# Performance work log

Hardware: AMD Instinct MI355X
Metric: run time of the kernel (lower is better)

The kernel has to match this reference:

```python
import jax, jax.numpy as jnp
import numpy as np

V, DW, DH, OUT = 50000, 300, 50, 4
B, T = 1024, 200


def setup_inputs() -> dict:
    key = jax.random.key(0)
    ks = jax.random.split(key, 9)
    x = jax.random.randint(ks[0], (B, T), 0, V)
    lengs = jax.random.randint(ks[1], (B,), 1, T + 1)  # valid lengths >= 1
    k = 1.0 / np.sqrt(DH)
    emb = jax.random.normal(ks[2], (V, DW), jnp.float32)
    emb = emb.at[0].set(0.0)  # padding_idx=0
    w_ih = jax.random.uniform(ks[3], (4 * DH, DW), jnp.float32, -k, k)
    w_hh = jax.random.uniform(ks[4], (4 * DH, DH), jnp.float32, -k, k)
    b_ih = jax.random.uniform(ks[5], (4 * DH,), jnp.float32, -k, k)
    b_hh = jax.random.uniform(ks[6], (4 * DH,), jnp.float32, -k, k)
    w_out = jax.random.uniform(ks[7], (OUT, DH), jnp.float32, -k, k)
    b_out = jax.random.uniform(ks[8], (OUT,), jnp.float32, -k, k)
    return {"x": x, "lengs": lengs, "emb": emb, "w_ih": w_ih, "w_hh": w_hh,
            "b_ih": b_ih, "b_hh": b_hh, "w_out": w_out, "b_out": b_out}


def reference(x, lengs, emb, w_ih, w_hh, b_ih, b_hh, w_out, b_out):
    b, t = x.shape
    xe = emb[x]                                        # [B,T,DW]
    mask = jnp.arange(t)[None, :] < lengs[:, None]     # [B,T] valid steps
    bias = b_ih + b_hh                                 # [4*DH]

    def step(carry, inp):
        h, c = carry
        x_t, m_t = inp                                 # [B,DW], [B]
        g = x_t @ w_ih.T + h @ w_hh.T + bias           # [B,4*DH]
        i, f, gg, o = jnp.split(g, 4, axis=-1)         # torch gate order i,f,g,o
        c_new = jax.nn.sigmoid(f) * c + jax.nn.sigmoid(i) * jnp.tanh(gg)
        h_new = jax.nn.sigmoid(o) * jnp.tanh(c_new)
        m = m_t[:, None]
        # packed-sequence semantics: state frozen past each sequence's length
        return (jnp.where(m, h_new, h), jnp.where(m, c_new, c)), None

    h0 = jnp.zeros((b, DH), xe.dtype)
    (h, _), _ = jax.lax.scan(step, (h0, h0),
                             (xe.transpose(1, 0, 2), mask.T))
    logits = h @ w_out.T + b_out                       # hidden.view(B,-1) -> Linear
    return jax.nn.softmax(logits, axis=1)
```

## Files before the change

kernel.cpp:

```cpp
#include <hip/hip_runtime.h>
#include <math.h>

#define VOCAB 50000
#define DW 300
#define DH 50
#define G4 200
#define BATCH 1024
#define TMAX 200
#define OUTC 4

__global__ __launch_bounds__(256) void transpose_wih(
    const float* __restrict__ w_ih, float* __restrict__ w_T)
{
    int i = blockIdx.x * 256 + threadIdx.x;
    if (i < G4 * DW) {
        int u = i / DW, k = i % DW;
        int u2 = (u % DH) * 4 + (u / DH);
        w_T[k * G4 + u2] = w_ih[i];
    }
}

__global__ __launch_bounds__(256, 2) void proj_kernel(
    const float* __restrict__ emb, const float* __restrict__ w_T,
    const float* __restrict__ b_ih, const float* __restrict__ b_hh,
    float* __restrict__ emb_proj)
{
    __shared__ __align__(16) float e_s[100 * 108];
    const int tid = threadIdx.x;
    const int v0 = blockIdx.x * 100;
    const int m_idx = tid / 25;
    const int n_idx = tid % 25;

    float acc[10][8];
#pragma unroll
    for (int m = 0; m < 10; m++)
#pragma unroll
        for (int c = 0; c < 8; c++) acc[m][c] = 0.f;

    const float* wcol = w_T + n_idx * 8;

    for (int kc = 0; kc < DW; kc += 100) {
        __syncthreads();
        for (int i = tid; i < 2500; i += 256) {
            int r = i / 25, c = i % 25;
            float4 v = *(const float4*)&emb[(size_t)(v0 + r) * DW + kc + c * 4];
            *(float4*)&e_s[r * 108 + c * 4] = v;
        }
        __syncthreads();

        if (tid < 250) {
            float4 wa[4], wb[4];
#pragma unroll
            for (int j = 0; j < 4; j++) {
                const float* p = wcol + (size_t)(kc + j) * G4;
                wa[j] = *(const float4*)p;
                wb[j] = *(const float4*)(p + 4);
            }
            for (int kk = 0; kk < 25; kk++) {
                float4 na[4], nb[4];
                int kn = kc + ((kk < 24) ? (kk + 1) : kk) * 4;
#pragma unroll
                for (int j = 0; j < 4; j++) {
                    const float* p = wcol + (size_t)(kn + j) * G4;
                    na[j] = *(const float4*)p;
                    nb[j] = *(const float4*)(p + 4);
                }
                float4 e4[10];
#pragma unroll
                for (int m = 0; m < 10; m++)
                    e4[m] = *(const float4*)&e_s[(m_idx * 10 + m) * 108 + kk * 4];
#pragma unroll
                for (int j = 0; j < 4; j++) {
#pragma unroll
                    for (int m = 0; m < 10; m++) {
                        float ev = (j == 0) ? e4[m].x : (j == 1) ? e4[m].y
                                 : (j == 2) ? e4[m].z : e4[m].w;
                        acc[m][0] = fmaf(ev, wa[j].x, acc[m][0]);
                        acc[m][1] = fmaf(ev, wa[j].y, acc[m][1]);
                        acc[m][2] = fmaf(ev, wa[j].z, acc[m][2]);
                        acc[m][3] = fmaf(ev, wa[j].w, acc[m][3]);
                        acc[m][4] = fmaf(ev, wb[j].x, acc[m][4]);
                        acc[m][5] = fmaf(ev, wb[j].y, acc[m][5]);
                        acc[m][6] = fmaf(ev, wb[j].z, acc[m][6]);
                        acc[m][7] = fmaf(ev, wb[j].w, acc[m][7]);
                    }
                }
#pragma unroll
                for (int j = 0; j < 4; j++) { wa[j] = na[j]; wb[j] = nb[j]; }
            }
        }
    }

    if (tid < 250) {
        float bias[8];
#pragma unroll
        for (int c = 0; c < 8; c++) {
            int u2 = n_idx * 8 + c;
            int u  = (u2 & 3) * DH + (u2 >> 2);
            bias[c] = b_ih[u] + b_hh[u];
        }
#pragma unroll
        for (int m = 0; m < 10; m++) {
            float* dst = &emb_proj[(size_t)(v0 + m_idx * 10 + m) * G4 + n_idx * 8];
            *(float4*)dst = make_float4(acc[m][0] + bias[0], acc[m][1] + bias[1],
                                        acc[m][2] + bias[2], acc[m][3] + bias[3]);
            *(float4*)(dst + 4) = make_float4(acc[m][4] + bias[4], acc[m][5] + bias[5],
                                              acc[m][6] + bias[6], acc[m][7] + bias[7]);
        }
    }
}

template <int CTRL>
__device__ __forceinline__ float qbcast(float x) {
    return __int_as_float(__builtin_amdgcn_update_dpp(
        0, __float_as_int(x), CTRL, 0xF, 0xF, true));
}

__global__ __launch_bounds__(256, 2) void lstm_kernel(
    const int* __restrict__ x, const int* __restrict__ lengs,
    const float* __restrict__ emb_proj, const float* __restrict__ w_hh,
    const float* __restrict__ w_out, const float* __restrict__ b_out,
    float* __restrict__ out)
{
    __shared__ __align__(16) float hbuf[2][52];
    __shared__ int x_s[TMAX];
    __shared__ float red[OUTC];

    const int tid  = threadIdx.x;
    const int b    = blockIdx.x;
    const int gate = tid & 3;
    const int unit = tid >> 2;
    const int uu   = (unit < DH) ? unit : DH - 1;
    const int col  = (tid < G4) ? tid : 0;
    const int len  = lengs[b];

    for (int i = tid; i < TMAX; i += 256) x_s[i] = x[b * TMAX + i];
    if (tid < 52) hbuf[0][tid] = 0.f;

    const float* wr = w_hh + (size_t)(gate * DH + uu) * DH;
#define LDW(J) ({ float2 ta_ = *(const float2*)(wr + 4 * (J));                \
                  float2 tb_ = *(const float2*)(wr + 4 * (J) + 2);            \
                  make_float4(ta_.x, ta_.y, tb_.x, tb_.y); })
    const float4 W0 = LDW(0),  W1 = LDW(1),  W2  = LDW(2),  W3  = LDW(3);
    const float4 W4 = LDW(4),  W5 = LDW(5),  W6  = LDW(6),  W7  = LDW(7);
    const float4 W8 = LDW(8),  W9 = LDW(9),  W10 = LDW(10), W11 = LDW(11);
    const float2 W12 = *(const float2*)(wr + 48);
#undef LDW

    __syncthreads();

    const float* ep = emb_proj;
    float p0 = ep[(size_t)x_s[0] * G4 + col];
    float p1 = ep[(size_t)x_s[1] * G4 + col];
    float p2 = ep[(size_t)x_s[2] * G4 + col];
    float c_reg = 0.f;

    for (int t = 0; t < len; t++) {
        float cur = p0; p0 = p1; p1 = p2;
        int nt = t + 3; nt = (nt < TMAX) ? nt : TMAX - 1;
        p2 = ep[(size_t)x_s[nt] * G4 + col];

        const float* hb = hbuf[t & 1];
        float4 h0  = *(const float4*)(hb + 0);
        float4 h1  = *(const float4*)(hb + 4);
        float4 h2  = *(const float4*)(hb + 8);
        float4 h3  = *(const float4*)(hb + 12);
        float4 h4  = *(const float4*)(hb + 16);
        float4 h5  = *(const float4*)(hb + 20);
        float4 h6  = *(const float4*)(hb + 24);
        float4 h7  = *(const float4*)(hb + 28);
        float4 h8  = *(const float4*)(hb + 32);
        float4 h9  = *(const float4*)(hb + 36);
        float4 h10 = *(const float4*)(hb + 40);
        float4 h11 = *(const float4*)(hb + 44);
        float2 h12 = *(const float2*)(hb + 48);

#define DOT4(A, H, W)                                                         \
        A = fmaf((H).x, (W).x, fmaf((H).y, (W).y,                             \
            fmaf((H).z, (W).z, fmaf((H).w, (W).w, A))));
        float a0 = cur, a1 = 0.f, a2 = 0.f, a3 = 0.f;
        DOT4(a0, h0, W0)  DOT4(a1, h1, W1)  DOT4(a2, h2,  W2)  DOT4(a3, h3,  W3)
        DOT4(a0, h4, W4)  DOT4(a1, h5, W5)  DOT4(a2, h6,  W6)  DOT4(a3, h7,  W7)
        DOT4(a0, h8, W8)  DOT4(a1, h9, W9)  DOT4(a2, h10, W10) DOT4(a3, h11, W11)
        a1 = fmaf(h12.x, W12.x, fmaf(h12.y, W12.y, a1));
#undef DOT4
        float g = (a0 + a1) + (a2 + a3);

        const bool isg = (gate == 2);
        float arg = isg ? (-2.f * g) : (-g);
        float r   = 1.f / (1.f + __expf(arg));
        float v   = isg ? fmaf(2.f, r, -1.f) : r;

        float si = qbcast<0x00>(v);
        float sf = qbcast<0x55>(v);
        float tc = qbcast<0xAA>(v);
        float so = qbcast<0xFF>(v);

        float cn = fmaf(sf, c_reg, si * tc);
        c_reg = cn;
        float th = fmaf(2.f, 1.f / (1.f + __expf(-2.f * cn)), -1.f);
        float hn = so * th;
        if ((gate == 0) && (tid < G4)) hbuf[(t + 1) & 1][unit] = hn;
        __syncthreads();
    }

    const float* hf = hbuf[len & 1];
    if (tid < OUTC) {
        float lg = b_out[tid];
        const float* wo = w_out + tid * DH;
#pragma unroll
        for (int k = 0; k < DH; k++) lg = fmaf(hf[k], wo[k], lg);
        red[tid] = lg;
    }
    if (tid < OUTC) {
        float m = fmaxf(fmaxf(red[0], red[1]), fmaxf(red[2], red[3]));
        float s = 0.f;
#pragma unroll
        for (int j = 0; j < OUTC; j++) s += __expf(red[j] - m);
        out[b * OUTC + tid] = __expf(red[tid] - m) / s;
    }
}

extern "C" void kernel_launch(void* const* d_in, const int* in_sizes, int n_in,
                              void* d_out, int out_size, void* d_ws, size_t ws_size,
                              hipStream_t stream) {
    const int*   x     = (const int*)d_in[0];
    const int*   lengs = (const int*)d_in[1];
    const float* emb   = (const float*)d_in[2];
    const float* w_ih  = (const float*)d_in[3];
    const float* w_hh  = (const float*)d_in[4];
    const float* b_ih  = (const float*)d_in[5];
    const float* b_hh  = (const float*)d_in[6];
    const float* w_out = (const float*)d_in[7];
    const float* b_out = (const float*)d_in[8];
    float* out = (float*)d_out;

    float* emb_proj = (float*)d_ws;
    float* w_T      = emb_proj + (size_t)VOCAB * G4;

    hipLaunchKernelGGL(transpose_wih, dim3((G4 * DW + 255) / 256), dim3(256),
                       0, stream, w_ih, w_T);
    hipLaunchKernelGGL(proj_kernel, dim3(VOCAB / 100), dim3(256), 0, stream,
                       emb, w_T, b_ih, b_hh, emb_proj);
    hipLaunchKernelGGL(lstm_kernel, dim3(BATCH), dim3(256), 0, stream,
                       x, lengs, emb_proj, w_hh, w_out, b_out, out);
}
```

Measured before the change: 347.5 us.

## Process four batch sequences per block with masked steps and padded W_hh rows

Each LSTM block now runs four sequences in lockstep up to the longest of the four lengths. Per-sequence masks freeze the cell and hidden state once a sequence has ended. A small new kernel copies W_hh into a 52-float padded row layout so each row loads as aligned float4s. The goal is to share one barrier per timestep across four sequences and to give each thread independent work it can overlap. In exchange, only a quarter as many blocks are launched, which lowers occupancy. Sequences shorter than the longest in their group also do wasted steps.

```diff
diff --git a/kernel.cpp b/kernel.cpp
--- a/kernel.cpp
+++ b/kernel.cpp
@@ -8,6 +8,7 @@
 #define BATCH 1024
 #define TMAX 200
 #define OUTC 4
+#define NB 4
 
 __global__ __launch_bounds__(256) void transpose_wih(
     const float* __restrict__ w_ih, float* __restrict__ w_T)
@@ -110,114 +111,156 @@
     }
 }
 
+__global__ __launch_bounds__(256) void prep_whh(
+    const float* __restrict__ w_hh, float* __restrict__ wp)
+{
+    int r = threadIdx.x;
+    if (r < G4) {
+        int gate = r & 3, unit = r >> 2;
+        const float* src = w_hh + (size_t)(gate * DH + unit) * DH;
+        float* dst = wp + r * 52;
+        for (int k = 0; k < DH; k++) dst[k] = src[k];
+        dst[50] = 0.f; dst[51] = 0.f;
+    }
+}
+
 template <int CTRL>
 __device__ __forceinline__ float qbcast(float x) {
     return __int_as_float(__builtin_amdgcn_update_dpp(
         0, __float_as_int(x), CTRL, 0xF, 0xF, true));
 }
 
-__global__ __launch_bounds__(256, 2) void lstm_kernel(
+__global__ __launch_bounds__(256) void lstm_kernel(
     const int* __restrict__ x, const int* __restrict__ lengs,
-    const float* __restrict__ emb_proj, const float* __restrict__ w_hh,
+    const float* __restrict__ emb_proj, const float* __restrict__ wp,
     const float* __restrict__ w_out, const float* __restrict__ b_out,
     float* __restrict__ out)
 {
-    __shared__ __align__(16) float hbuf[2][52];
-    __shared__ int x_s[TMAX];
-    __shared__ float red[OUTC];
+    __shared__ __align__(16) float hbuf[2][NB][52];
+    __shared__ int x_s[NB][TMAX];
+    __shared__ float red[NB][OUTC];
 
     const int tid  = threadIdx.x;
-    const int b    = blockIdx.x;
+    const int b4   = blockIdx.x * NB;
     const int gate = tid & 3;
     const int unit = tid >> 2;
-    const int uu   = (unit < DH) ? unit : DH - 1;
-    const int col  = (tid < G4) ? tid : 0;
-    const int len  = lengs[b];
-
-    for (int i = tid; i < TMAX; i += 256) x_s[i] = x[b * TMAX + i];
-    if (tid < 52) hbuf[0][tid] = 0.f;
-
-    const float* wr = w_hh + (size_t)(gate * DH + uu) * DH;
-#define LDW(J) ({ float2 ta_ = *(const float2*)(wr + 4 * (J));                \
-                  float2 tb_ = *(const float2*)(wr + 4 * (J) + 2);            \
-                  make_float4(ta_.x, ta_.y, tb_.x, tb_.y); })
-    const float4 W0 = LDW(0),  W1 = LDW(1),  W2  = LDW(2),  W3  = LDW(3);
-    const float4 W4 = LDW(4),  W5 = LDW(5),  W6  = LDW(6),  W7  = LDW(7);
-    const float4 W8 = LDW(8),  W9 = LDW(9),  W10 = LDW(10), W11 = LDW(11);
-    const float2 W12 = *(const float2*)(wr + 48);
-#undef LDW
+    const int row  = (tid < G4) ? tid : 0;
+
+    for (int i = tid; i < NB * TMAX; i += 256) {
+        int nb = i / TMAX, tt = i % TMAX;
+        x_s[nb][tt] = x[(size_t)(b4 + nb) * TMAX + tt];
+    }
+    for (int i = tid; i < 2 * NB * 52; i += 256) ((float*)hbuf)[i] = 0.f;
+
+    const int len0 = lengs[b4 + 0];
+    const int len1 = lengs[b4 + 1];
+    const int len2 = lengs[b4 + 2];
+    const int len3 = lengs[b4 + 3];
+    const int lenmax = max(max(len0, len1), max(len2, len3));
+
+    const float* wr = wp + (size_t)row * 52;
+    const float4 W0  = *(const float4*)(wr + 0);
+    const float4 W1  = *(const float4*)(wr + 4);
+    const float4 W2  = *(const float4*)(wr + 8);
+    const float4 W3  = *(const float4*)(wr + 12);
+    const float4 W4  = *(const float4*)(wr + 16);
+    const float4 W5  = *(const float4*)(wr + 20);
+    const float4 W6  = *(const float4*)(wr + 24);
+    const float4 W7  = *(const float4*)(wr + 28);
+    const float4 W8  = *(const float4*)(wr + 32);
+    const float4 W9  = *(const float4*)(wr + 36);
+    const float4 W10 = *(const float4*)(wr + 40);
+    const float4 W11 = *(const float4*)(wr + 44);
+    const float4 W12 = *(const float4*)(wr + 48);
 
     __syncthreads();
 
     const float* ep = emb_proj;
-    float p0 = ep[(size_t)x_s[0] * G4 + col];
-    float p1 = ep[(size_t)x_s[1] * G4 + col];
-    float p2 = ep[(size_t)x_s[2] * G4 + col];
-    float c_reg = 0.f;
-
-    for (int t = 0; t < len; t++) {
-        float cur = p0; p0 = p1; p1 = p2;
-        int nt = t + 3; nt = (nt < TMAX) ? nt : TMAX - 1;
-        p2 = ep[(size_t)x_s[nt] * G4 + col];
-
-        const float* hb = hbuf[t & 1];
-        float4 h0  = *(const float4*)(hb + 0);
-        float4 h1  = *(const float4*)(hb + 4);
-        float4 h2  = *(const float4*)(hb + 8);
-        float4 h3  = *(const float4*)(hb + 12);
-        float4 h4  = *(const float4*)(hb + 16);
-        float4 h5  = *(const float4*)(hb + 20);
-        float4 h6  = *(const float4*)(hb + 24);
-        float4 h7  = *(const float4*)(hb + 28);
-        float4 h8  = *(const float4*)(hb + 32);
-        float4 h9  = *(const float4*)(hb + 36);
-        float4 h10 = *(const float4*)(hb + 40);
-        float4 h11 = *(const float4*)(hb + 44);
-        float2 h12 = *(const float2*)(hb + 48);
+    float p00 = ep[(size_t)x_s[0][0] * G4 + row];
+    float p01 = ep[(size_t)x_s[0][1] * G4 + row];
+    float p10 = ep[(size_t)x_s[1][0] * G4 + row];
+    float p11 = ep[(size_t)x_s[1][1] * G4 + row];
+    float p20 = ep[(size_t)x_s[2][0] * G4 + row];
+    float p21 = ep[(size_t)x_s[2][1] * G4 + row];
+    float p30 = ep[(size_t)x_s[3][0] * G4 + row];
+    float p31 = ep[(size_t)x_s[3][1] * G4 + row];
+    float c0 = 0.f, c1 = 0.f, c2 = 0.f, c3 = 0.f;
+    float hp0 = 0.f, hp1 = 0.f, hp2 = 0.f, hp3 = 0.f;
 
 #define DOT4(A, H, W)                                                         \
         A = fmaf((H).x, (W).x, fmaf((H).y, (W).y,                             \
             fmaf((H).z, (W).z, fmaf((H).w, (W).w, A))));
-        float a0 = cur, a1 = 0.f, a2 = 0.f, a3 = 0.f;
-        DOT4(a0, h0, W0)  DOT4(a1, h1, W1)  DOT4(a2, h2,  W2)  DOT4(a3, h3,  W3)
-        DOT4(a0, h4, W4)  DOT4(a1, h5, W5)  DOT4(a2, h6,  W6)  DOT4(a3, h7,  W7)
-        DOT4(a0, h8, W8)  DOT4(a1, h9, W9)  DOT4(a2, h10, W10) DOT4(a3, h11, W11)
-        a1 = fmaf(h12.x, W12.x, fmaf(h12.y, W12.y, a1));
+
+#define STEP_ROW(R, pR0, pR1, cR, hpR, lenR)                                  \
+    {                                                                         \
+        float cur = pR0; pR0 = pR1;                                           \
+        pR1 = ep[(size_t)x_s[R][nt] * G4 + row];                              \
+        const float* hb = &hbuf[t & 1][R][0];                                 \
+        float4 h0  = *(const float4*)(hb + 0);                                \
+        float4 h1  = *(const float4*)(hb + 4);                                \
+        float4 h2  = *(const float4*)(hb + 8);                                \
+        float4 h3  = *(const float4*)(hb + 12);                               \
+        float4 h4  = *(const float4*)(hb + 16);                               \
+        float4 h5  = *(const float4*)(hb + 20);                               \
+        float4 h6  = *(const float4*)(hb + 24);                               \
+        float4 h7  = *(const float4*)(hb + 28);                               \
+        float4 h8  = *(const float4*)(hb + 32);                               \
+        float4 h9  = *(const float4*)(hb + 36);                               \
+        float4 h10 = *(const float4*)(hb + 40);                               \
+        float4 h11 = *(const float4*)(hb + 44);                               \
+        float4 h12 = *(const float4*)(hb + 48);                               \
+        float a0 = cur, a1 = 0.f, a2 = 0.f, a3 = 0.f;                         \
+        DOT4(a0, h0,  W0)  DOT4(a1, h1,  W1)                                  \
+        DOT4(a2, h2,  W2)  DOT4(a3, h3,  W3)                                  \
+        DOT4(a0, h4,  W4)  DOT4(a1, h5,  W5)                                  \
+        DOT4(a2, h6,  W6)  DOT4(a3, h7,  W7)                                  \
+        DOT4(a0, h8,  W8)  DOT4(a1, h9,  W9)                                  \
+        DOT4(a2, h10, W10) DOT4(a3, h11, W11)                                 \
+        DOT4(a0, h12, W12)                                                    \
+        float g = (a0 + a1) + (a2 + a3);                                      \
+        float y = (gate == 2) ? (-2.f * g) : (-g);                            \
+        float rr = 1.f / (1.f + __expf(y));                                   \
+        float v  = (gate == 2) ? fmaf(2.f, rr, -1.f) : rr;                    \
+        float si = qbcast<0x00>(v);                                           \
+        float sf = qbcast<0x55>(v);                                           \
+        float tc = qbcast<0xAA>(v);                                           \
+        float so = qbcast<0xFF>(v);                                           \
+        float cn = fmaf(sf, cR, si * tc);                                     \
+        bool live = (t < lenR);                                               \
+        cn = live ? cn : cR;                                                  \
+        cR = cn;                                                              \
+        float th = fmaf(2.f, 1.f / (1.f + __expf(-2.f * cn)), -1.f);          \
+        float hn = so * th;                                                   \
+        hn = live ? hn : hpR;                                                 \
+        hpR = hn;                                                             \
+        if ((gate == 0) && (tid < G4)) hbuf[(t + 1) & 1][R][unit] = hn;       \
+    }
+
+    for (int t = 0; t < lenmax; t++) {
+        int nt = (t + 2 < TMAX) ? (t + 2) : (TMAX - 1);
+        STEP_ROW(0, p00, p01, c0, hp0, len0)
+        STEP_ROW(1, p10, p11, c1, hp1, len1)
+        STEP_ROW(2, p20, p21, c2, hp2, len2)
+        STEP_ROW(3, p30, p31, c3, hp3, len3)
+        __syncthreads();
+    }
+#undef STEP_ROW
 #undef DOT4
-        float g = (a0 + a1) + (a2 + a3);
-
-        const bool isg = (gate == 2);
-        float arg = isg ? (-2.f * g) : (-g);
-        float r   = 1.f / (1.f + __expf(arg));
-        float v   = isg ? fmaf(2.f, r, -1.f) : r;
-
-        float si = qbcast<0x00>(v);
-        float sf = qbcast<0x55>(v);
-        float tc = qbcast<0xAA>(v);
-        float so = qbcast<0xFF>(v);
-
-        float cn = fmaf(sf, c_reg, si * tc);
-        c_reg = cn;
-        float th = fmaf(2.f, 1.f / (1.f + __expf(-2.f * cn)), -1.f);
-        float hn = so * th;
-        if ((gate == 0) && (tid < G4)) hbuf[(t + 1) & 1][unit] = hn;
-        __syncthreads();
-    }
-
-    const float* hf = hbuf[len & 1];
-    if (tid < OUTC) {
-        float lg = b_out[tid];
-        const float* wo = w_out + tid * DH;
+
+    if (tid < NB * OUTC) {
+        int nb = tid >> 2, o = tid & 3;
+        const float* hf = &hbuf[lenmax & 1][nb][0];
+        float lg = b_out[o];
+        const float* wo = w_out + o * DH;
 #pragma unroll
         for (int k = 0; k < DH; k++) lg = fmaf(hf[k], wo[k], lg);
-        red[tid] = lg;
-    }
-    if (tid < OUTC) {
-        float m = fmaxf(fmaxf(red[0], red[1]), fmaxf(red[2], red[3]));
+        red[nb][o] = lg;
+        float m = fmaxf(fmaxf(red[nb][0], red[nb][1]),
+                        fmaxf(red[nb][2], red[nb][3]));
         float s = 0.f;
 #pragma unroll
-        for (int j = 0; j < OUTC; j++) s += __expf(red[j] - m);
-        out[b * OUTC + tid] = __expf(red[tid] - m) / s;
+        for (int j = 0; j < OUTC; j++) s += __expf(red[nb][j] - m);
+        out[(size_t)(b4 + nb) * OUTC + o] = __expf(red[nb][o] - m) / s;
     }
 }
 
@@ -237,11 +280,13 @@
 
     float* emb_proj = (float*)d_ws;
     float* w_T      = emb_proj + (size_t)VOCAB * G4;
+    float* wp       = w_T;
 
     hipLaunchKernelGGL(transpose_wih, dim3((G4 * DW + 255) / 256), dim3(256),
                        0, stream, w_ih, w_T);
     hipLaunchKernelGGL(proj_kernel, dim3(VOCAB / 100), dim3(256), 0, stream,
                        emb, w_T, b_ih, b_hh, emb_proj);
-    hipLaunchKernelGGL(lstm_kernel, dim3(BATCH), dim3(256), 0, stream,
-                       x, lengs, emb_proj, w_hh, w_out, b_out, out);
-}
+    hipLaunchKernelGGL(prep_whh, dim3(1), dim3(256), 0, stream, w_hh, wp);
+    hipLaunchKernelGGL(lstm_kernel, dim3(BATCH / NB), dim3(256), 0, stream,
+                       x, lengs, emb_proj, wp, w_out, b_out, out);
+}
```

Measured after the change: 472.5 us. 36.0% more time.
